# Performance work log

Hardware: AMD Instinct MI355X
Metric: run time of the kernel (lower is better)

## Reference

```python
import jax, jax.numpy as jnp
from jax import lax
import numpy as np

B = 2; C = 128; H = 128; W = 128; NPIX = H * W
HTH = 184; HTW = 180; NBINS = HTH * HTW
NSPH = 16384; KHT = 8; KSPH = 16
N0, N1, N2 = 1024, 256, 64
K0, K1, K2 = 8, 8, 8
EPS = 1e-5


def setup_inputs() -> dict:
    key = jax.random.key(0)
    ks = jax.random.split(key, 24)
    f32 = jnp.float32
    inp = {}
    inp["image"] = jax.random.normal(ks[0], (B, C, H, W), f32)
    inp["bn_gamma"] = jnp.ones((C,), f32)
    inp["bn_beta"] = jnp.zeros((C,), f32)
    inp["ht_idx"] = jax.random.randint(ks[1], (NBINS, KHT), 0, NPIX, jnp.int32)
    inp["ht_w"] = jax.random.uniform(ks[2], (NBINS, KHT), f32)
    inp["w_htconv"] = jax.random.normal(ks[3], (3, 3, C, C), f32) / np.sqrt(9.0 * C)
    inp["htbn_gamma"] = jnp.ones((C,), f32)
    inp["htbn_beta"] = jnp.zeros((C,), f32)
    inp["sph_idx"] = jax.random.randint(ks[4], (NSPH, KSPH), 0, NBINS, jnp.int32)
    inp["sph_w"] = jax.random.uniform(ks[5], (NSPH, KSPH), f32)
    inp["w_sc"] = jax.random.normal(ks[6], (3, 64, C), f32) / np.sqrt(1.0 * C)
    inp["b_sc"] = jnp.zeros((3, 64), f32)
    inp["scbn_gamma"] = jnp.ones((3, 64), f32)
    inp["scbn_beta"] = jnp.zeros((3, 64), f32)
    inp["dgcn_w"] = jax.random.normal(ks[7], (3, 4, 128, 64), f32) / np.sqrt(128.0)
    inp["dgcn_b"] = jnp.zeros((3, 4, 64), f32)
    inp["dgcn_hw"] = jax.random.normal(ks[8], (3, 64), f32) / 8.0
    inp["dgcn_hb"] = jnp.zeros((3,), f32)
    inp["ind0"] = jax.random.randint(ks[9], (B, N0), 0, NSPH, jnp.int32)
    inp["ind1"] = jax.random.randint(ks[10], (B, 3, N1), 0, NSPH, jnp.int32)
    inp["ind2"] = jax.random.randint(ks[11], (B, 3, N2), 0, NSPH, jnp.int32)
    # kNN-style edges: structured centers (each node repeated k times), random neighbors
    c0 = jnp.tile(jnp.repeat(jnp.arange(N0, dtype=jnp.int32), K0)[None], (B, 1))
    inp["edge0"] = jnp.stack([c0, jax.random.randint(ks[12], (B, N0 * K0), 0, N0, jnp.int32)], 1)
    c1 = jnp.broadcast_to(jnp.repeat(jnp.arange(N1, dtype=jnp.int32), K1)[None, None], (B, 3, N1 * K1))
    inp["edge1"] = jnp.stack([c1, jax.random.randint(ks[13], (B, 3, N1 * K1), 0, N1, jnp.int32)], 2)
    c2 = jnp.broadcast_to(jnp.repeat(jnp.arange(N2, dtype=jnp.int32), K2)[None, None], (B, 3, N2 * K2))
    inp["edge2"] = jnp.stack([c2, jax.random.randint(ks[14], (B, 3, N2 * K2), 0, N2, jnp.int32)], 2)
    inp["target0"] = jax.random.randint(ks[15], (B, N0), 0, 2, jnp.int32)
    inp["target1"] = jax.random.randint(ks[16], (B * 3, N1), 0, 2, jnp.int32)
    inp["target2"] = jax.random.randint(ks[17], (B * 3, N2), 0, 2, jnp.int32)
    return inp


def _bn2d(x, g, b):
    m = x.mean((0, 2, 3), keepdims=True)
    v = x.var((0, 2, 3), keepdims=True)
    return g[None, :, None, None] * (x - m) * lax.rsqrt(v + EPS) + b[None, :, None, None]


def _sphere(x_htf, sph_idx, sph_w, ind):
    # x_htf: [B,C,NBINS]; ind: [B,S] -> weighted gather of HT bins per sphere node
    mi = sph_idx[ind]          # [B,S,K]
    mw = sph_w[ind]            # [B,S,K]
    g = jax.vmap(lambda xb, ib: xb[:, ib])(x_htf, mi)   # [B,C,S,K]
    return (g * mw[:, None]).sum(-1)                    # [B,C,S]


def _sconv(x, w, b, g, be):
    # 1x1 conv [B,C,S]->[B,64,S] + BN1d (batch stats) + ReLU
    y = jnp.einsum('oc,bcs->bos', w, x) + b[None, :, None]
    m = y.mean((0, 2), keepdims=True)
    v = y.var((0, 2), keepdims=True)
    return jax.nn.relu(g[None, :, None] * (y - m) * lax.rsqrt(v + EPS) + be[None, :, None])


def _dgcn(x, edge, ws, bs, hw, hb, n, k):
    # x: [Bg,n,64]; edge: [Bg,2,n*k] (row0=center, row1=neighbor); 4 EdgeConv layers
    for i in range(4):
        xc = jnp.take_along_axis(x, edge[:, 0, :, None], axis=1)   # [Bg,n*k,Cin]
        xn = jnp.take_along_axis(x, edge[:, 1, :, None], axis=1)
        h = jax.nn.relu(jnp.concatenate([xc, xn - xc], -1) @ ws[i] + bs[i])
        x = h.reshape(x.shape[0], n, k, -1).max(2)                 # max over neighbors
    return x @ hw + hb                                             # [Bg,n] logits


def _bce(logits, target):
    t = target.astype(logits.dtype)
    l = jnp.maximum(logits, 0.0) - logits * t + jnp.log1p(jnp.exp(-jnp.abs(logits)))
    pos = t > 0.5
    npos = jnp.maximum(pos.sum(), 1).astype(l.dtype)
    nneg = jnp.maximum((~pos).sum(), 1).astype(l.dtype)
    return jnp.where(pos, l, 0.0).sum() / npos, jnp.where(pos, 0.0, l).sum() / nneg


def _forward(image, bn_gamma, bn_beta, ht_idx, ht_w, w_htconv, htbn_gamma, htbn_beta,
             sph_idx, sph_w, w_sc, b_sc, scbn_gamma, scbn_beta,
             dgcn_w, dgcn_b, dgcn_hw, dgcn_hb,
             ind0, ind1, ind2, edge0, edge1, edge2, target0, target1, target2):
    x = jax.nn.relu(_bn2d(image, bn_gamma, bn_beta))
    xf = x.reshape(B, C, NPIX)
    # Hough voting: each HT bin accumulates KHT weighted pixels
    ht = (xf[:, :, ht_idx] * ht_w).sum(-1).reshape(B, C, HTH, HTW)
    hc = lax.conv_general_dilated(ht, w_htconv, (1, 1), 'SAME',
                                  dimension_numbers=('NCHW', 'HWIO', 'NCHW'))
    x_htf = jax.nn.relu(_bn2d(hc, htbn_gamma, htbn_beta)).reshape(B, C, NBINS)

    # scale 0
    x0 = _sconv(_sphere(x_htf, sph_idx, sph_w, ind0),
                w_sc[0], b_sc[0], scbn_gamma[0], scbn_beta[0]).transpose(0, 2, 1)
    x0 = _dgcn(x0, edge0, dgcn_w[0], dgcn_b[0], dgcn_hw[0], dgcn_hb[0], N0, K0)   # [B,N0]
    # scale 1 (3 vanishing-point branches folded into batch)
    x1 = _sconv(_sphere(x_htf, sph_idx, sph_w, ind1.reshape(B, -1)),
                w_sc[1], b_sc[1], scbn_gamma[1], scbn_beta[1]).transpose(0, 2, 1)
    x1 = _dgcn(x1.reshape(B * 3, N1, 64), edge1.reshape(B * 3, 2, N1 * K1),
               dgcn_w[1], dgcn_b[1], dgcn_hw[1], dgcn_hb[1], N1, K1)              # [B*3,N1]
    # scale 2
    x2 = _sconv(_sphere(x_htf, sph_idx, sph_w, ind2.reshape(B, -1)),
                w_sc[2], b_sc[2], scbn_gamma[2], scbn_beta[2]).transpose(0, 2, 1)
    x2 = _dgcn(x2.reshape(B * 3, N2, 64), edge2.reshape(B * 3, 2, N2 * K2),
               dgcn_w[2], dgcn_b[2], dgcn_hw[2], dgcn_hb[2], N2, K2)              # [B*3,N2]

    lp0, ln0 = _bce(x0, target0)
    lp1, ln1 = _bce(x1, target1)
    lp2, ln2 = _bce(x2, target2)
    losses = jnp.stack([lp0, ln0, lp1, ln1, lp2, ln2])
    preds = jnp.concatenate([jax.nn.sigmoid(x0).reshape(B, -1),
                             jax.nn.sigmoid(x1).reshape(B, -1),
                             jax.nn.sigmoid(x2).reshape(B, -1)], axis=1)
    return losses, preds


def reference(image, bn_gamma, bn_beta, ht_idx, ht_w, w_htconv, htbn_gamma, htbn_beta,
              sph_idx, sph_w, w_sc, b_sc, scbn_gamma, scbn_beta,
              dgcn_w, dgcn_b, dgcn_hw, dgcn_hb,
              ind0, ind1, ind2, edge0, edge1, edge2, target0, target1, target2):
    return _forward(image, bn_gamma, bn_beta, ht_idx, ht_w, w_htconv, htbn_gamma, htbn_beta,
                    sph_idx, sph_w, w_sc, b_sc, scbn_gamma, scbn_beta,
                    dgcn_w, dgcn_b, dgcn_hw, dgcn_hb,
                    ind0, ind1, ind2, edge0, edge1, edge2, target0, target1, target2)
```

## Files before the change

kernel.cpp:

```cpp
#include <hip/hip_runtime.h>
#include <math.h>

#define B_ 2
#define C_ 128
#define NPIX_ 16384
#define HTH_ 184
#define HTW_ 180
#define NBINS_ 33120
#define PH_ 186
#define PW_ 184
#define NPB_ 1984
#define TOTN_ 3968
#define EPS_ 1e-5f

#define ST_HC_SUM 0
#define ST_HC_SQ  128
#define ST_SC_SUM 256
#define ST_SC_SQ  448
#define ST_LOSS   640
#define ST_TICKET 652
#define ST_IMG_S1 1472
#define ST_IMG_S2 1600

typedef __attribute__((ext_vector_type(8))) short v8s;
typedef __attribute__((ext_vector_type(4))) float v4f;

__device__ inline unsigned short f2b(float f) {
  unsigned u = __builtin_bit_cast(unsigned, f);
  unsigned r = u + 0x7fffu + ((u >> 16) & 1u);
  return (unsigned short)(r >> 16);
}
__device__ inline float b2f(unsigned short u) {
  unsigned v = ((unsigned)u) << 16;
  return __builtin_bit_cast(float, v);
}

__global__ void kprep0(const float* __restrict__ w, const float* __restrict__ dw,
                       const float* __restrict__ wsc,
                       unsigned short* __restrict__ wtb, unsigned short* __restrict__ dwb,
                       unsigned short* __restrict__ swb,
                       unsigned* __restrict__ htb2, const float* __restrict__ img,
                       float* __restrict__ st) {
  int bid = blockIdx.x;
  int tid = threadIdx.x;
  if (bid < 1612) {
    int idx = bid*256 + tid;
    if (idx < 147456) {
      int tap = idx >> 14, z = idx & 16383;
      int j = z & 7, lane = (z >> 3) & 63, nt = (z >> 9) & 7, kt = (z >> 12) & 3;
      int l = lane & 15, q = lane >> 4;
      int co = nt*16 + l, ci = kt*32 + q*8 + j;
      wtb[idx] = f2b(w[(tap*C_ + ci)*C_ + co]);
    } else if (idx < 245760) {
      int i2 = idx - 147456;
      int sl = i2 >> 13, z = i2 & 8191;
      int j = z & 7, lane = (z >> 3) & 63, nt = (z >> 9) & 3, kt = (z >> 11) & 3;
      int l = lane & 15, q = lane >> 4;
      int co = nt*16 + l, cc = kt*32 + q*8 + j;
      dwb[i2] = f2b(dw[(sl*128 + cc)*64 + co]);
    } else if (idx < 270336) {
      int i3 = idx - 245760;
      int s = i3 >> 13, z = i3 & 8191;
      int j = z & 7, lane = (z >> 3) & 63, nt = (z >> 9) & 3, kt = (z >> 11) & 3;
      int l = lane & 15, q = lane >> 4;
      int co = nt*16 + l, cc = kt*32 + q*8 + j;
      swb[i3] = f2b(wsc[(s*64 + co)*128 + cc]);
    } else if (idx < 412672) {
      int i = idx - 270336;
      int d = i & 63;
      int cell = i >> 6;
      int b = cell / 1112, j = cell % 1112;
      int y, x;
      if (j < 184) { y = 0; x = j; }
      else if (j < 368) { y = 185; x = j - 184; }
      else { int c = j - 368; int xi = c / 186; y = c % 186; x = xi == 0 ? 0 : 180 + xi; }
      htb2[((size_t)(b*PH_ + y)*PW_ + x)*64 + d] = 0u;
    }
  } else {
    int kb = bid - 1612;
    int c = kb >> 3, chunk = kb & 7;
    float s1 = 0.f, s2 = 0.f;
    for (int i = chunk*4096 + tid; i < (chunk+1)*4096; i += 256) {
      int b = i >> 14, p = i & (NPIX_-1);
      float v = img[((size_t)(b*C_ + c))*NPIX_ + p];
      s1 += v; s2 += v*v;
    }
    __shared__ float r1[256], r2[256];
    r1[tid] = s1; r2[tid] = s2; __syncthreads();
    for (int off = 128; off; off >>= 1) {
      if (tid < off) { r1[tid] += r1[tid+off]; r2[tid] += r2[tid+off]; }
      __syncthreads();
    }
    if (tid == 0) {
      atomicAdd(&st[ST_IMG_S1 + c], r1[0]);
      atomicAdd(&st[ST_IMG_S2 + c], r2[0]);
    }
  }
}

__global__ void k2_bnrelu_t(const float* __restrict__ img, const float* __restrict__ st,
                            const float* __restrict__ g, const float* __restrict__ be,
                            unsigned short* __restrict__ xt) {
  __shared__ float tile[32*65];
  __shared__ float ash[32], dsh[32];
  int p0 = blockIdx.x*64, c0 = blockIdx.y*32, b = blockIdx.z;
  int tid = threadIdx.x;
  if (tid < 32) {
    int c = c0 + tid;
    float n = (float)(B_*NPIX_);
    float m = st[ST_IMG_S1+c]/n;
    float var = st[ST_IMG_S2+c]/n - m*m;
    float a = g[c]*rsqrtf(var + EPS_);
    ash[tid] = a; dsh[tid] = be[c] - a*m;
  }
  __syncthreads();
  for (int r = 0; r < 8; r++) {
    int flat = tid + r*256;
    int row = flat >> 6, col = flat & 63;
    float v = img[((size_t)(b*C_ + c0 + row))*NPIX_ + p0 + col];
    tile[row*65 + col] = fmaxf(ash[row]*v + dsh[row], 0.f);
  }
  __syncthreads();
  for (int r = 0; r < 4; r++) {
    int flat = (tid + r*256)*2;
    int pl = flat >> 5, cl = flat & 31;
    unsigned lo = f2b(tile[cl*65 + pl]);
    unsigned hi = f2b(tile[(cl+1)*65 + pl]);
    *(unsigned*)&xt[((size_t)b*NPIX_ + p0 + pl)*C_ + c0 + cl] = lo | (hi << 16);
  }
}

__global__ void k3_hough(const unsigned* __restrict__ xt2, const int* __restrict__ hidx,
                         const float* __restrict__ hwt, unsigned* __restrict__ htb2) {
  int tid = threadIdx.x;
  int wv = __builtin_amdgcn_readfirstlane(tid >> 6);
  int lane = tid & 63;
  int b = blockIdx.y;
  int bin0 = blockIdx.x*16 + wv*4;
  const unsigned* base = xt2 + (size_t)b*NPIX_*64 + lane;
  unsigned dv[4][8];
  #pragma unroll
  for (int i = 0; i < 4; i++) {
    #pragma unroll
    for (int k = 0; k < 8; k++) {
      int p = hidx[(bin0+i)*8 + k];
      dv[i][k] = base[(size_t)p*64];
    }
  }
  #pragma unroll
  for (int i = 0; i < 4; i++) {
    int bin = bin0 + i;
    float acc0 = 0.f, acc1 = 0.f;
    #pragma unroll
    for (int k = 0; k < 8; k++) {
      float w = hwt[bin*8 + k];
      acc0 += w * b2f((unsigned short)(dv[i][k] & 0xffff));
      acc1 += w * b2f((unsigned short)(dv[i][k] >> 16));
    }
    int y = bin / HTW_, x = bin - y*HTW_;
    htb2[((size_t)(b*PH_ + y + 1)*PW_ + (x+1))*64 + lane] =
        (unsigned)f2b(acc0) | (((unsigned)f2b(acc1)) << 16);
  }
}

__global__ __launch_bounds__(256, 3) void k4_mfma(
    const unsigned short* __restrict__ htb, const unsigned short* __restrict__ wtb,
    unsigned short* __restrict__ hcb, float* __restrict__ st) {
  __shared__ char smem[32768];
  int tid = threadIdx.x;
  int wav = tid >> 6, lane = tid & 63;
  int quad = lane >> 4, l16 = lane & 15;
  int b = blockIdx.y;
  int p0 = blockIdx.x*128 + wav*32;
  size_t ab[2];
  #pragma unroll
  for (int t = 0; t < 2; t++) {
    int px = p0 + t*16 + l16; if (px > NBINS_-1) px = NBINS_-1;
    int y = px / HTW_, x = px % HTW_;
    ab[t] = (((size_t)(b*PH_ + y))*PW_ + x)*C_ + quad*8;
  }
  v4f acc[2][8];
  #pragma unroll
  for (int t = 0; t < 2; t++)
    #pragma unroll
    for (int nt = 0; nt < 8; nt++) acc[t][nt] = (v4f){0,0,0,0};

  for (int tap = 0; tap < 9; tap++) {
    __syncthreads();
    const uint4* src = (const uint4*)(wtb + tap*16384);
    uint4* dst = (uint4*)smem;
    #pragma unroll
    for (int s = 0; s < 8; s++) dst[tid + s*256] = src[tid + s*256];
    __syncthreads();
    int dy = tap/3, dx = tap - dy*3;
    int toff = (dy*PW_ + dx)*C_;
    v8s a[2][4];
    #pragma unroll
    for (int t = 0; t < 2; t++)
      #pragma unroll
      for (int kt = 0; kt < 4; kt++)
        a[t][kt] = *(const v8s*)&htb[ab[t] + toff + kt*32];
    #pragma unroll
    for (int kt = 0; kt < 4; kt++) {
      #pragma unroll
      for (int nt = 0; nt < 8; nt++) {
        v8s bf = *(const v8s*)(smem + ((((kt*8 + nt)*64) + lane) << 4));
        acc[0][nt] = __builtin_amdgcn_mfma_f32_16x16x32_bf16(a[0][kt], bf, acc[0][nt], 0, 0, 0);
        acc[1][nt] = __builtin_amdgcn_mfma_f32_16x16x32_bf16(a[1][kt], bf, acc[1][nt], 0, 0, 0);
      }
    }
  }
  __syncthreads();
  float* red = (float*)smem;
  float s1[8], s2[8];
  #pragma unroll
  for (int nt = 0; nt < 8; nt++) { s1[nt] = 0.f; s2[nt] = 0.f; }
  #pragma unroll
  for (int t = 0; t < 2; t++) {
    int pbase = p0 + t*16 + quad*4;
    #pragma unroll
    for (int nt = 0; nt < 8; nt++) {
      int co = nt*16 + l16;
      #pragma unroll
      for (int reg = 0; reg < 4; reg++) {
        int po = pbase + reg;
        if (po < NBINS_) {
          float v = acc[t][nt][reg];
          hcb[((size_t)b*NBINS_ + po)*C_ + co] = f2b(v);
          s1[nt] += v; s2[nt] += v*v;
        }
      }
    }
  }
  int slot = wav*4 + quad;
  #pragma unroll
  for (int nt = 0; nt < 8; nt++) red[(nt*16 + l16)*17 + slot] = s1[nt];
  __syncthreads();
  if (tid < 128) {
    float s = 0.f;
    #pragma unroll
    for (int k = 0; k < 16; k++) s += red[tid*17 + k];
    atomicAdd(&st[ST_HC_SUM + tid], s);
  }
  __syncthreads();
  #pragma unroll
  for (int nt = 0; nt < 8; nt++) red[(nt*16 + l16)*17 + slot] = s2[nt];
  __syncthreads();
  if (tid < 128) {
    float s = 0.f;
    #pragma unroll
    for (int k = 0; k < 16; k++) s += red[tid*17 + k];
    atomicAdd(&st[ST_HC_SQ + tid], s);
  }
}

__global__ __launch_bounds__(256) void k67_sphconv(
    const unsigned* __restrict__ hcb2, const float* __restrict__ g, const float* __restrict__ be,
    const int* __restrict__ sph_idx, const float* __restrict__ sph_w,
    const int* __restrict__ ind0, const int* __restrict__ ind1, const int* __restrict__ ind2,
    const unsigned short* __restrict__ swb, const float* __restrict__ b_sc,
    float* __restrict__ y, float* __restrict__ st) {
  __shared__ unsigned short E[16*136];
  int tid = threadIdx.x;
  int gn0 = blockIdx.x*8;
  int nb0 = gn0 % NPB_;
  int s = nb0 < 1024 ? 0 : (nb0 < 1792 ? 1 : 2);
  int wv = tid >> 6, lane = tid & 63;
  int quad = lane >> 4, l16 = lane & 15;
  {
    int c0 = lane*2, c1 = c0 + 1;
    float n = (float)(B_*NBINS_);
    float m0 = st[ST_HC_SUM + c0]/n, m1 = st[ST_HC_SUM + c1]/n;
    float va0 = st[ST_HC_SQ + c0]/n - m0*m0, va1 = st[ST_HC_SQ + c1]/n - m1*m1;
    float a0 = g[c0]*rsqrtf(va0 + EPS_), a1 = g[c1]*rsqrtf(va1 + EPS_);
    float d0 = be[c0] - a0*m0, d1 = be[c1] - a1*m1;
    #pragma unroll
    for (int i = 0; i < 2; i++) {
      int node_l = wv*2 + i;
      int gn = gn0 + node_l;
      int b = gn / NPB_, nb = gn % NPB_;
      int v;
      if (nb < 1024) v = ind0[b*1024 + nb];
      else if (nb < 1792) v = ind1[b*768 + nb - 1024];
      else v = ind2[b*192 + nb - 1792];
      v = __builtin_amdgcn_readfirstlane(v);
      const unsigned* base = hcb2 + (size_t)b*NBINS_*64 + lane;
      float acc0 = 0.f, acc1 = 0.f;
      #pragma unroll
      for (int k = 0; k < 16; k++) {
        int mi = sph_idx[v*16 + k];
        float mw = sph_w[v*16 + k];
        unsigned dv = base[(size_t)mi*64];
        acc0 += mw * fmaxf(a0*b2f((unsigned short)(dv & 0xffff)) + d0, 0.f);
        acc1 += mw * fmaxf(a1*b2f((unsigned short)(dv >> 16)) + d1, 0.f);
      }
      unsigned lo = f2b(acc0), hi = f2b(acc1);
      *(unsigned*)&E[node_l*136 + c0] = lo | (hi << 16);
    }
  }
  __syncthreads();
  v4f acc = (v4f){0,0,0,0};
  const unsigned short* wb = swb + s*8192 + wv*512;
  #pragma unroll
  for (int kt = 0; kt < 4; kt++) {
    v8s a = *(const v8s*)&E[l16*136 + quad*8 + kt*32];
    v8s bf = *(const v8s*)&wb[kt*2048 + lane*8];
    acc = __builtin_amdgcn_mfma_f32_16x16x32_bf16(a, bf, acc, 0, 0, 0);
  }
  float bias = b_sc[s*64 + wv*16 + l16];
  float s1 = 0.f, s2 = 0.f;
  #pragma unroll
  for (int reg = 0; reg < 4; reg++) {
    int row = quad*4 + reg;
    if (quad < 2) {
      float val = acc[reg] + bias;
      y[(size_t)(gn0 + row)*64 + wv*16 + l16] = val;
      s1 += val; s2 += val*val;
    }
  }
  s1 += __shfl_xor(s1, 16);
  s2 += __shfl_xor(s2, 16);
  if (quad == 0) {
    atomicAdd(&st[ST_SC_SUM + s*64 + wv*16 + l16], s1);
    atomicAdd(&st[ST_SC_SQ  + s*64 + wv*16 + l16], s2);
  }
}

__global__ __launch_bounds__(256) void k10_dgcn(
    const void* __restrict__ xin_, unsigned short* __restrict__ xout,
    const int* __restrict__ edge0, const int* __restrict__ edge1, const int* __restrict__ edge2,
    const unsigned short* __restrict__ dwb, const float* __restrict__ db,
    const float* __restrict__ st, const float* __restrict__ scg, const float* __restrict__ scb,
    int layer, int usebn) {
  __shared__ unsigned short E[64*136];
  __shared__ float ash[64], dsh[64];
  int tid = threadIdx.x;
  int bid = blockIdx.x;
  int s, node_base, le_blk, span; const int* ec;
  if (bid < 256) {
    s = 0; int b = bid >> 7; node_base = b*NPB_; le_blk = (bid & 127)*64;
    span = 8192; ec = edge0 + b*2*8192;
  } else if (bid < 448) {
    int j = bid - 256; s = 1; int seg = j >> 5; int b = seg/3, vp = seg%3;
    node_base = b*NPB_ + 1024 + vp*256; le_blk = (j & 31)*64;
    span = 2048; ec = edge1 + ((b*3+vp)*2)*2048;
  } else {
    int j = bid - 448; s = 2; int seg = j >> 3; int b = seg/3, vp = seg%3;
    node_base = b*NPB_ + 1792 + vp*64; le_blk = (j & 7)*64;
    span = 512; ec = edge2 + ((b*3+vp)*2)*512;
  }
  const int* en = ec + span;
  if (usebn) {
    if (tid < 64) {
      float n = s==0 ? 2048.f : (s==1 ? 1536.f : 384.f);
      float m = st[ST_SC_SUM + s*64 + tid]/n;
      float var = st[ST_SC_SQ + s*64 + tid]/n - m*m;
      float a = scg[s*64 + tid]*rsqrtf(var + EPS_);
      ash[tid] = a; dsh[tid] = scb[s*64 + tid] - a*m;
    }
    __syncthreads();
  }
  {
    int e_l = tid >> 2, part = tid & 3;
    int h = part >> 1, cb = (part & 1)*32;
    int e = le_blk + e_l;
    int ci = ec[e], ni = en[e];
    if (usebn) {
      const float* xc = (const float*)xin_ + (size_t)(node_base + ci)*64 + cb;
      const float* xn = (const float*)xin_ + (size_t)(node_base + ni)*64 + cb;
      float4 xc4[8], xn4[8];
      #pragma unroll
      for (int q = 0; q < 8; q++) xc4[q] = *(const float4*)&xc[q*4];
      if (h) {
        #pragma unroll
        for (int q = 0; q < 8; q++) xn4[q] = *(const float4*)&xn[q*4];
      }
      #pragma unroll
      for (int c8 = 0; c8 < 32; c8 += 8) {
        v8s pk;
        #pragma unroll
        for (int j = 0; j < 8; j++) {
          int cl = c8 + j;
          int c = cb + cl;
          float xcv = ((const float*)xc4)[cl];
          float vc = fmaxf(ash[c]*xcv + dsh[c], 0.f);
          float val = vc;
          if (h) {
            float xnv = ((const float*)xn4)[cl];
            val = fmaxf(ash[c]*xnv + dsh[c], 0.f) - vc;
          }
          pk[j] = (short)f2b(val);
        }
        *(v8s*)&E[e_l*136 + h*64 + cb + c8] = pk;
      }
    } else {
      const unsigned short* xc = (const unsigned short*)xin_ + (size_t)(node_base + ci)*64 + cb;
      const unsigned short* xn = (const unsigned short*)xin_ + (size_t)(node_base + ni)*64 + cb;
      #pragma unroll
      for (int c8 = 0; c8 < 32; c8 += 8) {
        v8s vc8 = *(const v8s*)&xc[c8];
        v8s pk = vc8;
        if (h) {
          v8s vn8 = *(const v8s*)&xn[c8];
          #pragma unroll
          for (int j = 0; j < 8; j++)
            pk[j] = (short)f2b(b2f((unsigned short)vn8[j]) - b2f((unsigned short)vc8[j]));
        }
        *(v8s*)&E[e_l*136 + h*64 + cb + c8] = pk;
      }
    }
  }
  __syncthreads();
  int wave = tid >> 6, lane = tid & 63;
  int quad = lane >> 4, l16 = lane & 15;
  const unsigned short* wb = dwb + (size_t)(s*4 + layer)*8192;
  v4f acc[4];
  #pragma unroll
  for (int nt = 0; nt < 4; nt++) acc[nt] = (v4f){0,0,0,0};
  #pragma unroll
  for (int kt = 0; kt < 4; kt++) {
    v8s a = *(const v8s*)&E[(wave*16 + l16)*136 + quad*8 + kt*32];
    #pragma unroll
    for (int nt = 0; nt < 4; nt++) {
      v8s bf = *(const v8s*)&wb[((kt*4 + nt)*64 + lane)*8];
      acc[nt] = __builtin_amdgcn_mfma_f32_16x16x32_bf16(a, bf, acc[nt], 0, 0, 0);
    }
  }
  #pragma unroll
  for (int nt = 0; nt < 4; nt++) {
    float bias = db[(s*4 + layer)*64 + nt*16 + l16];
    float m = fmaxf(fmaxf(acc[nt][0], acc[nt][1]), fmaxf(acc[nt][2], acc[nt][3]));
    m = fmaxf(m + bias, 0.f);
    float other = __shfl_xor(m, 16);
    m = fmaxf(m, other);
    if ((quad & 1) == 0) {
      int node_l = wave*2 + (quad >> 1);
      xout[(size_t)(node_base + (le_blk >> 3) + node_l)*64 + nt*16 + l16] = f2b(m);
    }
  }
}

__global__ __launch_bounds__(256) void k11_head(
    const unsigned short* __restrict__ x, const float* __restrict__ hw, const float* __restrict__ hb,
    const int* __restrict__ t0, const int* __restrict__ t1, const int* __restrict__ t2,
    float* __restrict__ out, float* __restrict__ st) {
  __shared__ float shw[192];
  int tid = threadIdx.x;
  if (tid < 192) shw[tid] = hw[tid];
  __syncthreads();
  int gn = blockIdx.x*256 + tid;
  bool valid = gn < TOTN_;
  int g = valid ? gn : TOTN_-1;
  int b = g / NPB_, nb = g % NPB_;
  int s, tg;
  if (nb < 1024) { s = 0; tg = t0[b*1024 + nb]; }
  else if (nb < 1792) { s = 1; int j = nb-1024; tg = t1[(b*3 + (j>>8))*256 + (j&255)]; }
  else { s = 2; int j = nb-1792; tg = t2[(b*3 + (j>>6))*64 + (j&63)]; }
  const unsigned short* row = x + (size_t)g*64;
  float logit = hb[s];
  #pragma unroll
  for (int c8 = 0; c8 < 64; c8 += 8) {
    v8s v = *(const v8s*)&row[c8];
    #pragma unroll
    for (int j = 0; j < 8; j++)
      logit += b2f((unsigned short)v[j]) * shw[s*64 + c8 + j];
  }
  if (valid) out[6 + gn] = 1.f / (1.f + expf(-logit));
  float tf = (float)tg;
  float l = fmaxf(logit, 0.f) - logit*tf + log1pf(expf(-fabsf(logit)));
  float sp = (valid && tg) ? l : 0.f;
  float sn = (valid && !tg) ? l : 0.f;
  float cp = (valid && tg) ? 1.f : 0.f;
  float cn = (valid && !tg) ? 1.f : 0.f;
  for (int off = 32; off; off >>= 1) {
    sp += __shfl_down(sp, off);
    sn += __shfl_down(sn, off);
    cp += __shfl_down(cp, off);
    cn += __shfl_down(cn, off);
  }
  if ((tid & 63) == 0) {
    atomicAdd(&st[ST_LOSS + s*4 + 0], sp);
    atomicAdd(&st[ST_LOSS + s*4 + 1], sn);
    atomicAdd(&st[ST_LOSS + s*4 + 2], cp);
    atomicAdd(&st[ST_LOSS + s*4 + 3], cn);
  }
  __syncthreads();
  __threadfence();
  if (tid == 0) {
    unsigned t = (unsigned)atomicAdd(&st[ST_TICKET], 1.f);
    if (t >= 15) {
      #pragma unroll
      for (int i = 0; i < 6; i++) {
        int sc = i >> 1; int pos = !(i & 1);
        float sum = atomicAdd(&st[ST_LOSS + sc*4 + (pos ? 0 : 1)], 0.f);
        float cnt = atomicAdd(&st[ST_LOSS + sc*4 + (pos ? 2 : 3)], 0.f);
        out[i] = sum / fmaxf(cnt, 1.f);
      }
    }
  }
}

extern "C" void kernel_launch(void* const* d_in, const int* in_sizes, int n_in,
                              void* d_out, int out_size, void* d_ws, size_t ws_size,
                              hipStream_t stream) {
  const float* image  = (const float*)d_in[0];
  const float* bn_g   = (const float*)d_in[1];
  const float* bn_b   = (const float*)d_in[2];
  const int*   ht_idx = (const int*)  d_in[3];
  const float* ht_w   = (const float*)d_in[4];
  const float* w_conv = (const float*)d_in[5];
  const float* htbn_g = (const float*)d_in[6];
  const float* htbn_b = (const float*)d_in[7];
  const int*   sph_idx= (const int*)  d_in[8];
  const float* sph_w  = (const float*)d_in[9];
  const float* w_sc   = (const float*)d_in[10];
  const float* b_sc   = (const float*)d_in[11];
  const float* scbn_g = (const float*)d_in[12];
  const float* scbn_b = (const float*)d_in[13];
  const float* dgcn_w = (const float*)d_in[14];
  const float* dgcn_b = (const float*)d_in[15];
  const float* dgcn_hw= (const float*)d_in[16];
  const float* dgcn_hb= (const float*)d_in[17];
  const int*   ind0   = (const int*)  d_in[18];
  const int*   ind1   = (const int*)  d_in[19];
  const int*   ind2   = (const int*)  d_in[20];
  const int*   edge0  = (const int*)  d_in[21];
  const int*   edge1  = (const int*)  d_in[22];
  const int*   edge2  = (const int*)  d_in[23];
  const int*   t0     = (const int*)  d_in[24];
  const int*   t1     = (const int*)  d_in[25];
  const int*   t2     = (const int*)  d_in[26];
  float* out = (float*)d_out;

  char* ws = (char*)d_ws;
  unsigned short* x_t   = (unsigned short*)(ws);
  unsigned short* htb   = (unsigned short*)(ws +  8388608);
  unsigned short* hcb   = (unsigned short*)(ws + 25911296);
  unsigned short* wtb   = (unsigned short*)(ws + 42868736);
  unsigned short* dwb   = (unsigned short*)(ws + 43163648);
  unsigned short* swb   = (unsigned short*)(ws + 43360256);
  float*          y_sc  = (float*)(ws + 43409408);
  unsigned short* xdgA  = (unsigned short*)(ws + 44425216);
  unsigned short* xdgB  = (unsigned short*)(ws + 44933120);
  float*          st    = (float*)(ws + 45441024);

  hipMemsetAsync(st, 0, 1728*sizeof(float), stream);
  kprep0<<<2636, 256, 0, stream>>>(w_conv, dgcn_w, w_sc, wtb, dwb, swb, (unsigned*)htb, image, st);
  k2_bnrelu_t<<<dim3(256,4,2), 256, 0, stream>>>(image, st, bn_g, bn_b, x_t);
  k3_hough<<<dim3(NBINS_/16, B_), 256, 0, stream>>>((const unsigned*)x_t, ht_idx, ht_w, (unsigned*)htb);
  k4_mfma<<<dim3(259, 2), 256, 0, stream>>>(htb, wtb, hcb, st);
  k67_sphconv<<<TOTN_/8, 256, 0, stream>>>((const unsigned*)hcb, htbn_g, htbn_b, sph_idx, sph_w,
                                           ind0, ind1, ind2, swb, b_sc, y_sc, st);
  k10_dgcn<<<496, 256, 0, stream>>>((const void*)y_sc, xdgA, edge0, edge1, edge2, dwb, dgcn_b, st, scbn_g, scbn_b, 0, 1);
  k10_dgcn<<<496, 256, 0, stream>>>((const void*)xdgA, xdgB, edge0, edge1, edge2, dwb, dgcn_b, st, scbn_g, scbn_b, 1, 0);
  k10_dgcn<<<496, 256, 0, stream>>>((const void*)xdgB, xdgA, edge0, edge1, edge2, dwb, dgcn_b, st, scbn_g, scbn_b, 2, 0);
  k10_dgcn<<<496, 256, 0, stream>>>((const void*)xdgA, xdgB, edge0, edge1, edge2, dwb, dgcn_b, st, scbn_g, scbn_b, 3, 0);
  k11_head<<<16, 256, 0, stream>>>(xdgB, dgcn_hw, dgcn_hb, t0, t1, t2, out, st);
}
```

Baseline: 239.3 us.

## Fuse sphere conv, DGCN layers and head into one persistent kernel with grid barriers

New measurement: 725.5 us. 3.03x slower.

```diff
diff --git a/kernel.cpp b/kernel.cpp
--- a/kernel.cpp
+++ b/kernel.cpp
@@ -19,8 +19,9 @@
 #define ST_SC_SQ  448
 #define ST_LOSS   640
 #define ST_TICKET 652
-#define ST_IMG_S1 1472
-#define ST_IMG_S2 1600
+#define ST_BAR    656
+#define ST_IMG_P1 704
+#define ST_IMG_P2 1728
 
 typedef __attribute__((ext_vector_type(8))) short v8s;
 typedef __attribute__((ext_vector_type(4))) float v4f;
@@ -33,6 +34,18 @@
 __device__ inline float b2f(unsigned short u) {
   unsigned v = ((unsigned)u) << 16;
   return __builtin_bit_cast(float, v);
+}
+
+__device__ inline void gbar(int* bar, int idx, int nb) {
+  __syncthreads();
+  __threadfence();
+  if (threadIdx.x == 0) {
+    __hip_atomic_fetch_add(&bar[idx], 1, __ATOMIC_ACQ_REL, __HIP_MEMORY_SCOPE_AGENT);
+    while (__hip_atomic_load(&bar[idx], __ATOMIC_ACQUIRE, __HIP_MEMORY_SCOPE_AGENT) < nb)
+      __builtin_amdgcn_s_sleep(1);
+  }
+  __syncthreads();
+  __threadfence();
 }
 
 __global__ void kprep0(const float* __restrict__ w, const float* __restrict__ dw,
@@ -76,7 +89,7 @@
       else { int c = j - 368; int xi = c / 186; y = c % 186; x = xi == 0 ? 0 : 180 + xi; }
       htb2[((size_t)(b*PH_ + y)*PW_ + x)*64 + d] = 0u;
     }
-  } else {
+  } else if (bid < 2636) {
     int kb = bid - 1612;
     int c = kb >> 3, chunk = kb & 7;
     float s1 = 0.f, s2 = 0.f;
@@ -92,9 +105,11 @@
       __syncthreads();
     }
     if (tid == 0) {
-      atomicAdd(&st[ST_IMG_S1 + c], r1[0]);
-      atomicAdd(&st[ST_IMG_S2 + c], r2[0]);
-    }
+      st[ST_IMG_P1 + chunk*128 + c] = r1[0];
+      st[ST_IMG_P2 + chunk*128 + c] = r2[0];
+    }
+  } else {
+    for (int i = tid; i < 672; i += 256) st[i] = 0.f;
   }
 }
 
@@ -107,9 +122,15 @@
   int tid = threadIdx.x;
   if (tid < 32) {
     int c = c0 + tid;
+    float s1 = 0.f, s2 = 0.f;
+    #pragma unroll
+    for (int ch = 0; ch < 8; ch++) {
+      s1 += st[ST_IMG_P1 + ch*128 + c];
+      s2 += st[ST_IMG_P2 + ch*128 + c];
+    }
     float n = (float)(B_*NPIX_);
-    float m = st[ST_IMG_S1+c]/n;
-    float var = st[ST_IMG_S2+c]/n - m*m;
+    float m = s1/n;
+    float var = s2/n - m*m;
     float a = g[c]*rsqrtf(var + EPS_);
     ash[tid] = a; dsh[tid] = be[c] - a*m;
   }
@@ -163,15 +184,16 @@
   }
 }
 
-__global__ __launch_bounds__(256, 3) void k4_mfma(
+__global__ __launch_bounds__(256, 4) void k4_mfma(
     const unsigned short* __restrict__ htb, const unsigned short* __restrict__ wtb,
     unsigned short* __restrict__ hcb, float* __restrict__ st) {
   __shared__ char smem[32768];
   int tid = threadIdx.x;
   int wav = tid >> 6, lane = tid & 63;
   int quad = lane >> 4, l16 = lane & 15;
+  int ph = wav & 1, ch = wav >> 1;
   int b = blockIdx.y;
-  int p0 = blockIdx.x*128 + wav*32;
+  int p0 = blockIdx.x*64 + ph*32;
   size_t ab[2];
   #pragma unroll
   for (int t = 0; t < 2; t++) {
@@ -179,11 +201,11 @@
     int y = px / HTW_, x = px % HTW_;
     ab[t] = (((size_t)(b*PH_ + y))*PW_ + x)*C_ + quad*8;
   }
-  v4f acc[2][8];
+  v4f acc[2][4];
   #pragma unroll
   for (int t = 0; t < 2; t++)
     #pragma unroll
-    for (int nt = 0; nt < 8; nt++) acc[t][nt] = (v4f){0,0,0,0};
+    for (int nt = 0; nt < 4; nt++) acc[t][nt] = (v4f){0,0,0,0};
 
   for (int tap = 0; tap < 9; tap++) {
     __syncthreads();
@@ -203,8 +225,8 @@
     #pragma unroll
     for (int kt = 0; kt < 4; kt++) {
       #pragma unroll
-      for (int nt = 0; nt < 8; nt++) {
-        v8s bf = *(const v8s*)(smem + ((((kt*8 + nt)*64) + lane) << 4));
+      for (int nt = 0; nt < 4; nt++) {
+        v8s bf = *(const v8s*)(smem + ((((kt*8 + ch*4 + nt)*64) + lane) << 4));
         acc[0][nt] = __builtin_amdgcn_mfma_f32_16x16x32_bf16(a[0][kt], bf, acc[0][nt], 0, 0, 0);
         acc[1][nt] = __builtin_amdgcn_mfma_f32_16x16x32_bf16(a[1][kt], bf, acc[1][nt], 0, 0, 0);
       }
@@ -212,15 +234,13 @@
   }
   __syncthreads();
   float* red = (float*)smem;
-  float s1[8], s2[8];
-  #pragma unroll
-  for (int nt = 0; nt < 8; nt++) { s1[nt] = 0.f; s2[nt] = 0.f; }
+  float s1[4] = {0,0,0,0}, s2[4] = {0,0,0,0};
   #pragma unroll
   for (int t = 0; t < 2; t++) {
     int pbase = p0 + t*16 + quad*4;
     #pragma unroll
-    for (int nt = 0; nt < 8; nt++) {
-      int co = nt*16 + l16;
+    for (int nt = 0; nt < 4; nt++) {
+      int co = ch*64 + nt*16 + l16;
       #pragma unroll
       for (int reg = 0; reg < 4; reg++) {
         int po = pbase + reg;
@@ -232,110 +252,111 @@
       }
     }
   }
-  int slot = wav*4 + quad;
-  #pragma unroll
-  for (int nt = 0; nt < 8; nt++) red[(nt*16 + l16)*17 + slot] = s1[nt];
+  int slot = ph*4 + quad;
+  #pragma unroll
+  for (int nt = 0; nt < 4; nt++) red[(ch*64 + nt*16 + l16)*9 + slot] = s1[nt];
   __syncthreads();
   if (tid < 128) {
     float s = 0.f;
     #pragma unroll
-    for (int k = 0; k < 16; k++) s += red[tid*17 + k];
+    for (int k = 0; k < 8; k++) s += red[tid*9 + k];
     atomicAdd(&st[ST_HC_SUM + tid], s);
   }
   __syncthreads();
   #pragma unroll
-  for (int nt = 0; nt < 8; nt++) red[(nt*16 + l16)*17 + slot] = s2[nt];
+  for (int nt = 0; nt < 4; nt++) red[(ch*64 + nt*16 + l16)*9 + slot] = s2[nt];
   __syncthreads();
   if (tid < 128) {
     float s = 0.f;
     #pragma unroll
-    for (int k = 0; k < 16; k++) s += red[tid*17 + k];
+    for (int k = 0; k < 8; k++) s += red[tid*9 + k];
     atomicAdd(&st[ST_HC_SQ + tid], s);
   }
 }
 
-__global__ __launch_bounds__(256) void k67_sphconv(
+__global__ __launch_bounds__(256, 2) void kmega(
     const unsigned* __restrict__ hcb2, const float* __restrict__ g, const float* __restrict__ be,
     const int* __restrict__ sph_idx, const float* __restrict__ sph_w,
     const int* __restrict__ ind0, const int* __restrict__ ind1, const int* __restrict__ ind2,
     const unsigned short* __restrict__ swb, const float* __restrict__ b_sc,
-    float* __restrict__ y, float* __restrict__ st) {
-  __shared__ unsigned short E[16*136];
-  int tid = threadIdx.x;
-  int gn0 = blockIdx.x*8;
-  int nb0 = gn0 % NPB_;
-  int s = nb0 < 1024 ? 0 : (nb0 < 1792 ? 1 : 2);
-  int wv = tid >> 6, lane = tid & 63;
-  int quad = lane >> 4, l16 = lane & 15;
-  {
-    int c0 = lane*2, c1 = c0 + 1;
-    float n = (float)(B_*NBINS_);
-    float m0 = st[ST_HC_SUM + c0]/n, m1 = st[ST_HC_SUM + c1]/n;
-    float va0 = st[ST_HC_SQ + c0]/n - m0*m0, va1 = st[ST_HC_SQ + c1]/n - m1*m1;
-    float a0 = g[c0]*rsqrtf(va0 + EPS_), a1 = g[c1]*rsqrtf(va1 + EPS_);
-    float d0 = be[c0] - a0*m0, d1 = be[c1] - a1*m1;
-    #pragma unroll
-    for (int i = 0; i < 2; i++) {
-      int node_l = wv*2 + i;
-      int gn = gn0 + node_l;
-      int b = gn / NPB_, nb = gn % NPB_;
-      int v;
-      if (nb < 1024) v = ind0[b*1024 + nb];
-      else if (nb < 1792) v = ind1[b*768 + nb - 1024];
-      else v = ind2[b*192 + nb - 1792];
-      v = __builtin_amdgcn_readfirstlane(v);
-      const unsigned* base = hcb2 + (size_t)b*NBINS_*64 + lane;
-      float acc0 = 0.f, acc1 = 0.f;
-      #pragma unroll
-      for (int k = 0; k < 16; k++) {
-        int mi = sph_idx[v*16 + k];
-        float mw = sph_w[v*16 + k];
-        unsigned dv = base[(size_t)mi*64];
-        acc0 += mw * fmaxf(a0*b2f((unsigned short)(dv & 0xffff)) + d0, 0.f);
-        acc1 += mw * fmaxf(a1*b2f((unsigned short)(dv >> 16)) + d1, 0.f);
-      }
-      unsigned lo = f2b(acc0), hi = f2b(acc1);
-      *(unsigned*)&E[node_l*136 + c0] = lo | (hi << 16);
-    }
-  }
-  __syncthreads();
-  v4f acc = (v4f){0,0,0,0};
-  const unsigned short* wb = swb + s*8192 + wv*512;
-  #pragma unroll
-  for (int kt = 0; kt < 4; kt++) {
-    v8s a = *(const v8s*)&E[l16*136 + quad*8 + kt*32];
-    v8s bf = *(const v8s*)&wb[kt*2048 + lane*8];
-    acc = __builtin_amdgcn_mfma_f32_16x16x32_bf16(a, bf, acc, 0, 0, 0);
-  }
-  float bias = b_sc[s*64 + wv*16 + l16];
-  float s1 = 0.f, s2 = 0.f;
-  #pragma unroll
-  for (int reg = 0; reg < 4; reg++) {
-    int row = quad*4 + reg;
-    if (quad < 2) {
-      float val = acc[reg] + bias;
-      y[(size_t)(gn0 + row)*64 + wv*16 + l16] = val;
-      s1 += val; s2 += val*val;
-    }
-  }
-  s1 += __shfl_xor(s1, 16);
-  s2 += __shfl_xor(s2, 16);
-  if (quad == 0) {
-    atomicAdd(&st[ST_SC_SUM + s*64 + wv*16 + l16], s1);
-    atomicAdd(&st[ST_SC_SQ  + s*64 + wv*16 + l16], s2);
-  }
-}
-
-__global__ __launch_bounds__(256) void k10_dgcn(
-    const void* __restrict__ xin_, unsigned short* __restrict__ xout,
     const int* __restrict__ edge0, const int* __restrict__ edge1, const int* __restrict__ edge2,
     const unsigned short* __restrict__ dwb, const float* __restrict__ db,
-    const float* __restrict__ st, const float* __restrict__ scg, const float* __restrict__ scb,
-    int layer, int usebn) {
+    const float* __restrict__ scg, const float* __restrict__ scb,
+    const float* __restrict__ hw, const float* __restrict__ hb,
+    const int* __restrict__ t0, const int* __restrict__ t1, const int* __restrict__ t2,
+    float* __restrict__ y_sc, unsigned short* __restrict__ xdgA, unsigned short* __restrict__ xdgB,
+    float* __restrict__ out, float* __restrict__ st) {
   __shared__ unsigned short E[64*136];
   __shared__ float ash[64], dsh[64];
   int tid = threadIdx.x;
   int bid = blockIdx.x;
+  int* bar = (int*)&st[ST_BAR];
+  int wv = tid >> 6, lane = tid & 63;
+  int quad = lane >> 4, l16 = lane & 15;
+
+  {
+    int gn0 = bid*8;
+    int nb0 = gn0 % NPB_;
+    int s = nb0 < 1024 ? 0 : (nb0 < 1792 ? 1 : 2);
+    {
+      int c0 = lane*2, c1 = c0 + 1;
+      float n = (float)(B_*NBINS_);
+      float m0 = st[ST_HC_SUM + c0]/n, m1 = st[ST_HC_SUM + c1]/n;
+      float va0 = st[ST_HC_SQ + c0]/n - m0*m0, va1 = st[ST_HC_SQ + c1]/n - m1*m1;
+      float a0 = g[c0]*rsqrtf(va0 + EPS_), a1 = g[c1]*rsqrtf(va1 + EPS_);
+      float d0 = be[c0] - a0*m0, d1 = be[c1] - a1*m1;
+      #pragma unroll
+      for (int i = 0; i < 2; i++) {
+        int node_l = wv*2 + i;
+        int gn = gn0 + node_l;
+        int b = gn / NPB_, nb = gn % NPB_;
+        int v;
+        if (nb < 1024) v = ind0[b*1024 + nb];
+        else if (nb < 1792) v = ind1[b*768 + nb - 1024];
+        else v = ind2[b*192 + nb - 1792];
+        v = __builtin_amdgcn_readfirstlane(v);
+        const unsigned* base = hcb2 + (size_t)b*NBINS_*64 + lane;
+        float acc0 = 0.f, acc1 = 0.f;
+        #pragma unroll
+        for (int k = 0; k < 16; k++) {
+          int mi = sph_idx[v*16 + k];
+          float mw = sph_w[v*16 + k];
+          unsigned dv = base[(size_t)mi*64];
+          acc0 += mw * fmaxf(a0*b2f((unsigned short)(dv & 0xffff)) + d0, 0.f);
+          acc1 += mw * fmaxf(a1*b2f((unsigned short)(dv >> 16)) + d1, 0.f);
+        }
+        unsigned lo = f2b(acc0), hi = f2b(acc1);
+        *(unsigned*)&E[node_l*136 + c0] = lo | (hi << 16);
+      }
+    }
+    __syncthreads();
+    v4f acc = (v4f){0,0,0,0};
+    const unsigned short* wb = swb + s*8192 + wv*512;
+    #pragma unroll
+    for (int kt = 0; kt < 4; kt++) {
+      v8s a = *(const v8s*)&E[l16*136 + quad*8 + kt*32];
+      v8s bf = *(const v8s*)&wb[kt*2048 + lane*8];
+      acc = __builtin_amdgcn_mfma_f32_16x16x32_bf16(a, bf, acc, 0, 0, 0);
+    }
+    float bias = b_sc[s*64 + wv*16 + l16];
+    float s1 = 0.f, s2 = 0.f;
+    #pragma unroll
+    for (int reg = 0; reg < 4; reg++) {
+      int row = quad*4 + reg;
+      if (quad < 2) {
+        float val = acc[reg] + bias;
+        y_sc[(size_t)(gn0 + row)*64 + wv*16 + l16] = val;
+        s1 += val; s2 += val*val;
+      }
+    }
+    s1 += __shfl_xor(s1, 16);
+    s2 += __shfl_xor(s2, 16);
+    if (quad == 0) {
+      atomicAdd(&st[ST_SC_SUM + s*64 + wv*16 + l16], s1);
+      atomicAdd(&st[ST_SC_SQ  + s*64 + wv*16 + l16], s2);
+    }
+  }
+
   int s, node_base, le_blk, span; const int* ec;
   if (bid < 256) {
     s = 0; int b = bid >> 7; node_base = b*NPB_; le_blk = (bid & 127)*64;
@@ -350,151 +371,158 @@
     span = 512; ec = edge2 + ((b*3+vp)*2)*512;
   }
   const int* en = ec + span;
-  if (usebn) {
-    if (tid < 64) {
-      float n = s==0 ? 2048.f : (s==1 ? 1536.f : 384.f);
-      float m = st[ST_SC_SUM + s*64 + tid]/n;
-      float var = st[ST_SC_SQ + s*64 + tid]/n - m*m;
-      float a = scg[s*64 + tid]*rsqrtf(var + EPS_);
-      ash[tid] = a; dsh[tid] = scb[s*64 + tid] - a*m;
-    }
-    __syncthreads();
-  }
+
+  for (int layer = 0; layer < 4; layer++) {
+    gbar(bar, layer, 496);
+    if (layer == 0) {
+      if (tid < 64) {
+        float n = s==0 ? 2048.f : (s==1 ? 1536.f : 384.f);
+        float m = st[ST_SC_SUM + s*64 + tid]/n;
+        float var = st[ST_SC_SQ + s*64 + tid]/n - m*m;
+        float a = scg[s*64 + tid]*rsqrtf(var + EPS_);
+        ash[tid] = a; dsh[tid] = scb[s*64 + tid] - a*m;
+      }
+      __syncthreads();
+    }
+    const void* xin_ = layer == 0 ? (const void*)y_sc
+                     : (layer == 1 ? (const void*)xdgA
+                     : (layer == 2 ? (const void*)xdgB : (const void*)xdgA));
+    unsigned short* xout = (layer & 1) ? xdgB : xdgA;
+    if (layer == 2) xout = xdgA; else if (layer == 0) xout = xdgA; else xout = xdgB;
+    {
+      int e_l = tid >> 2, part = tid & 3;
+      int h = part >> 1, cb = (part & 1)*32;
+      int e = le_blk + e_l;
+      int ci = ec[e], ni = en[e];
+      if (layer == 0) {
+        const float* xc = (const float*)xin_ + (size_t)(node_base + ci)*64 + cb;
+        const float* xn = (const float*)xin_ + (size_t)(node_base + ni)*64 + cb;
+        float4 xc4[8], xn4[8];
+        #pragma unroll
+        for (int q = 0; q < 8; q++) xc4[q] = *(const float4*)&xc[q*4];
+        if (h) {
+          #pragma unroll
+          for (int q = 0; q < 8; q++) xn4[q] = *(const float4*)&xn[q*4];
+        }
+        #pragma unroll
+        for (int c8 = 0; c8 < 32; c8 += 8) {
+          v8s pk;
+          #pragma unroll
+          for (int j = 0; j < 8; j++) {
+            int cl = c8 + j;
+            int c = cb + cl;
+            float xcv = ((const float*)xc4)[cl];
+            float vc = fmaxf(ash[c]*xcv + dsh[c], 0.f);
+            float val = vc;
+            if (h) {
+              float xnv = ((const float*)xn4)[cl];
+              val = fmaxf(ash[c]*xnv + dsh[c], 0.f) - vc;
+            }
+            pk[j] = (short)f2b(val);
+          }
+          *(v8s*)&E[e_l*136 + h*64 + cb + c8] = pk;
+        }
+      } else {
+        const unsigned short* xc = (const unsigned short*)xin_ + (size_t)(node_base + ci)*64 + cb;
+        const unsigned short* xn = (const unsigned short*)xin_ + (size_t)(node_base + ni)*64 + cb;
+        #pragma unroll
+        for (int c8 = 0; c8 < 32; c8 += 8) {
+          v8s vc8 = *(const v8s*)&xc[c8];
+          v8s pk = vc8;
+          if (h) {
+            v8s vn8 = *(const v8s*)&xn[c8];
+            #pragma unroll
+            for (int j = 0; j < 8; j++)
+              pk[j] = (short)f2b(b2f((unsigned short)vn8[j]) - b2f((unsigned short)vc8[j]));
+          }
+          *(v8s*)&E[e_l*136 + h*64 + cb + c8] = pk;
+        }
+      }
+    }
+    __syncthreads();
+    const unsigned short* wb = dwb + (size_t)(s*4 + layer)*8192;
+    v4f acc[4];
+    #pragma unroll
+    for (int nt = 0; nt < 4; nt++) acc[nt] = (v4f){0,0,0,0};
+    #pragma unroll
+    for (int kt = 0; kt < 4; kt++) {
+      v8s a = *(const v8s*)&E[(wv*16 + l16)*136 + quad*8 + kt*32];
+      #pragma unroll
+      for (int nt = 0; nt < 4; nt++) {
+        v8s bf = *(const v8s*)&wb[((kt*4 + nt)*64 + lane)*8];
+        acc[nt] = __builtin_amdgcn_mfma_f32_16x16x32_bf16(a, bf, acc[nt], 0, 0, 0);
+      }
+    }
+    #pragma unroll
+    for (int nt = 0; nt < 4; nt++) {
+      float bias = db[(s*4 + layer)*64 + nt*16 + l16];
+      float m = fmaxf(fmaxf(acc[nt][0], acc[nt][1]), fmaxf(acc[nt][2], acc[nt][3]));
+      m = fmaxf(m + bias, 0.f);
+      float other = __shfl_xor(m, 16);
+      m = fmaxf(m, other);
+      if ((quad & 1) == 0) {
+        int node_l = wv*2 + (quad >> 1);
+        xout[(size_t)(node_base + (le_blk >> 3) + node_l)*64 + nt*16 + l16] = f2b(m);
+      }
+    }
+    __syncthreads();
+  }
+
+  gbar(bar, 4, 496);
+  if (bid >= 16) return;
+
   {
-    int e_l = tid >> 2, part = tid & 3;
-    int h = part >> 1, cb = (part & 1)*32;
-    int e = le_blk + e_l;
-    int ci = ec[e], ni = en[e];
-    if (usebn) {
-      const float* xc = (const float*)xin_ + (size_t)(node_base + ci)*64 + cb;
-      const float* xn = (const float*)xin_ + (size_t)(node_base + ni)*64 + cb;
-      float4 xc4[8], xn4[8];
+    __shared__ float shw[192];
+    if (tid < 192) shw[tid] = hw[tid];
+    __syncthreads();
+    int gn = bid*256 + tid;
+    bool valid = gn < TOTN_;
+    int gg = valid ? gn : TOTN_-1;
+    int b = gg / NPB_, nb = gg % NPB_;
+    int sc_, tg;
+    if (nb < 1024) { sc_ = 0; tg = t0[b*1024 + nb]; }
+    else if (nb < 1792) { sc_ = 1; int j = nb-1024; tg = t1[(b*3 + (j>>8))*256 + (j&255)]; }
+    else { sc_ = 2; int j = nb-1792; tg = t2[(b*3 + (j>>6))*64 + (j&63)]; }
+    const unsigned short* row = xdgB + (size_t)gg*64;
+    float logit = hb[sc_];
+    #pragma unroll
+    for (int c8 = 0; c8 < 64; c8 += 8) {
+      v8s v = *(const v8s*)&row[c8];
       #pragma unroll
-      for (int q = 0; q < 8; q++) xc4[q] = *(const float4*)&xc[q*4];
-      if (h) {
+      for (int j = 0; j < 8; j++)
+        logit += b2f((unsigned short)v[j]) * shw[sc_*64 + c8 + j];
+    }
+    if (valid) out[6 + gn] = 1.f / (1.f + expf(-logit));
+    float tf = (float)tg;
+    float l = fmaxf(logit, 0.f) - logit*tf + log1pf(expf(-fabsf(logit)));
+    float sp = (valid && tg) ? l : 0.f;
+    float sn = (valid && !tg) ? l : 0.f;
+    float cp = (valid && tg) ? 1.f : 0.f;
+    float cn = (valid && !tg) ? 1.f : 0.f;
+    for (int off = 32; off; off >>= 1) {
+      sp += __shfl_down(sp, off);
+      sn += __shfl_down(sn, off);
+      cp += __shfl_down(cp, off);
+      cn += __shfl_down(cn, off);
+    }
+    if ((tid & 63) == 0) {
+      atomicAdd(&st[ST_LOSS + sc_*4 + 0], sp);
+      atomicAdd(&st[ST_LOSS + sc_*4 + 1], sn);
+      atomicAdd(&st[ST_LOSS + sc_*4 + 2], cp);
+      atomicAdd(&st[ST_LOSS + sc_*4 + 3], cn);
+    }
+    __syncthreads();
+    __threadfence();
+    if (tid == 0) {
+      unsigned t = (unsigned)atomicAdd(&st[ST_TICKET], 1.f);
+      if (t >= 15) {
         #pragma unroll
-        for (int q = 0; q < 8; q++) xn4[q] = *(const float4*)&xn[q*4];
-      }
-      #pragma unroll
-      for (int c8 = 0; c8 < 32; c8 += 8) {
-        v8s pk;
-        #pragma unroll
-        for (int j = 0; j < 8; j++) {
-          int cl = c8 + j;
-          int c = cb + cl;
-          float xcv = ((const float*)xc4)[cl];
-          float vc = fmaxf(ash[c]*xcv + dsh[c], 0.f);
-          float val = vc;
-          if (h) {
-            float xnv = ((const float*)xn4)[cl];
-            val = fmaxf(ash[c]*xnv + dsh[c], 0.f) - vc;
-          }
-          pk[j] = (short)f2b(val);
+        for (int i = 0; i < 6; i++) {
+          int sc2 = i >> 1; int pos = !(i & 1);
+          float sum = atomicAdd(&st[ST_LOSS + sc2*4 + (pos ? 0 : 1)], 0.f);
+          float cnt = atomicAdd(&st[ST_LOSS + sc2*4 + (pos ? 2 : 3)], 0.f);
+          out[i] = sum / fmaxf(cnt, 1.f);
         }
-        *(v8s*)&E[e_l*136 + h*64 + cb + c8] = pk;
-      }
-    } else {
-      const unsigned short* xc = (const unsigned short*)xin_ + (size_t)(node_base + ci)*64 + cb;
-      const unsigned short* xn = (const unsigned short*)xin_ + (size_t)(node_base + ni)*64 + cb;
-      #pragma unroll
-      for (int c8 = 0; c8 < 32; c8 += 8) {
-        v8s vc8 = *(const v8s*)&xc[c8];
-        v8s pk = vc8;
-        if (h) {
-          v8s vn8 = *(const v8s*)&xn[c8];
-          #pragma unroll
-          for (int j = 0; j < 8; j++)
-            pk[j] = (short)f2b(b2f((unsigned short)vn8[j]) - b2f((unsigned short)vc8[j]));
-        }
-        *(v8s*)&E[e_l*136 + h*64 + cb + c8] = pk;
-      }
-    }
-  }
-  __syncthreads();
-  int wave = tid >> 6, lane = tid & 63;
-  int quad = lane >> 4, l16 = lane & 15;
-  const unsigned short* wb = dwb + (size_t)(s*4 + layer)*8192;
-  v4f acc[4];
-  #pragma unroll
-  for (int nt = 0; nt < 4; nt++) acc[nt] = (v4f){0,0,0,0};
-  #pragma unroll
-  for (int kt = 0; kt < 4; kt++) {
-    v8s a = *(const v8s*)&E[(wave*16 + l16)*136 + quad*8 + kt*32];
-    #pragma unroll
-    for (int nt = 0; nt < 4; nt++) {
-      v8s bf = *(const v8s*)&wb[((kt*4 + nt)*64 + lane)*8];
-      acc[nt] = __builtin_amdgcn_mfma_f32_16x16x32_bf16(a, bf, acc[nt], 0, 0, 0);
-    }
-  }
-  #pragma unroll
-  for (int nt = 0; nt < 4; nt++) {
-    float bias = db[(s*4 + layer)*64 + nt*16 + l16];
-    float m = fmaxf(fmaxf(acc[nt][0], acc[nt][1]), fmaxf(acc[nt][2], acc[nt][3]));
-    m = fmaxf(m + bias, 0.f);
-    float other = __shfl_xor(m, 16);
-    m = fmaxf(m, other);
-    if ((quad & 1) == 0) {
-      int node_l = wave*2 + (quad >> 1);
-      xout[(size_t)(node_base + (le_blk >> 3) + node_l)*64 + nt*16 + l16] = f2b(m);
-    }
-  }
-}
-
-__global__ __launch_bounds__(256) void k11_head(
-    const unsigned short* __restrict__ x, const float* __restrict__ hw, const float* __restrict__ hb,
-    const int* __restrict__ t0, const int* __restrict__ t1, const int* __restrict__ t2,
-    float* __restrict__ out, float* __restrict__ st) {
-  __shared__ float shw[192];
-  int tid = threadIdx.x;
-  if (tid < 192) shw[tid] = hw[tid];
-  __syncthreads();
-  int gn = blockIdx.x*256 + tid;
-  bool valid = gn < TOTN_;
-  int g = valid ? gn : TOTN_-1;
-  int b = g / NPB_, nb = g % NPB_;
-  int s, tg;
-  if (nb < 1024) { s = 0; tg = t0[b*1024 + nb]; }
-  else if (nb < 1792) { s = 1; int j = nb-1024; tg = t1[(b*3 + (j>>8))*256 + (j&255)]; }
-  else { s = 2; int j = nb-1792; tg = t2[(b*3 + (j>>6))*64 + (j&63)]; }
-  const unsigned short* row = x + (size_t)g*64;
-  float logit = hb[s];
-  #pragma unroll
-  for (int c8 = 0; c8 < 64; c8 += 8) {
-    v8s v = *(const v8s*)&row[c8];
-    #pragma unroll
-    for (int j = 0; j < 8; j++)
-      logit += b2f((unsigned short)v[j]) * shw[s*64 + c8 + j];
-  }
-  if (valid) out[6 + gn] = 1.f / (1.f + expf(-logit));
-  float tf = (float)tg;
-  float l = fmaxf(logit, 0.f) - logit*tf + log1pf(expf(-fabsf(logit)));
-  float sp = (valid && tg) ? l : 0.f;
-  float sn = (valid && !tg) ? l : 0.f;
-  float cp = (valid && tg) ? 1.f : 0.f;
-  float cn = (valid && !tg) ? 1.f : 0.f;
-  for (int off = 32; off; off >>= 1) {
-    sp += __shfl_down(sp, off);
-    sn += __shfl_down(sn, off);
-    cp += __shfl_down(cp, off);
-    cn += __shfl_down(cn, off);
-  }
-  if ((tid & 63) == 0) {
-    atomicAdd(&st[ST_LOSS + s*4 + 0], sp);
-    atomicAdd(&st[ST_LOSS + s*4 + 1], sn);
-    atomicAdd(&st[ST_LOSS + s*4 + 2], cp);
-    atomicAdd(&st[ST_LOSS + s*4 + 3], cn);
-  }
-  __syncthreads();
-  __threadfence();
-  if (tid == 0) {
-    unsigned t = (unsigned)atomicAdd(&st[ST_TICKET], 1.f);
-    if (t >= 15) {
-      #pragma unroll
-      for (int i = 0; i < 6; i++) {
-        int sc = i >> 1; int pos = !(i & 1);
-        float sum = atomicAdd(&st[ST_LOSS + sc*4 + (pos ? 0 : 1)], 0.f);
-        float cnt = atomicAdd(&st[ST_LOSS + sc*4 + (pos ? 2 : 3)], 0.f);
-        out[i] = sum / fmaxf(cnt, 1.f);
       }
     }
   }
@@ -544,16 +572,13 @@
   unsigned short* xdgB  = (unsigned short*)(ws + 44933120);
   float*          st    = (float*)(ws + 45441024);
 
-  hipMemsetAsync(st, 0, 1728*sizeof(float), stream);
-  kprep0<<<2636, 256, 0, stream>>>(w_conv, dgcn_w, w_sc, wtb, dwb, swb, (unsigned*)htb, image, st);
+  kprep0<<<2637, 256, 0, stream>>>(w_conv, dgcn_w, w_sc, wtb, dwb, swb, (unsigned*)htb, image, st);
   k2_bnrelu_t<<<dim3(256,4,2), 256, 0, stream>>>(image, st, bn_g, bn_b, x_t);
   k3_hough<<<dim3(NBINS_/16, B_), 256, 0, stream>>>((const unsigned*)x_t, ht_idx, ht_w, (unsigned*)htb);
-  k4_mfma<<<dim3(259, 2), 256, 0, stream>>>(htb, wtb, hcb, st);
-  k67_sphconv<<<TOTN_/8, 256, 0, stream>>>((const unsigned*)hcb, htbn_g, htbn_b, sph_idx, sph_w,
-                                           ind0, ind1, ind2, swb, b_sc, y_sc, st);
-  k10_dgcn<<<496, 256, 0, stream>>>((const void*)y_sc, xdgA, edge0, edge1, edge2, dwb, dgcn_b, st, scbn_g, scbn_b, 0, 1);
-  k10_dgcn<<<496, 256, 0, stream>>>((const void*)xdgA, xdgB, edge0, edge1, edge2, dwb, dgcn_b, st, scbn_g, scbn_b, 1, 0);
-  k10_dgcn<<<496, 256, 0, stream>>>((const void*)xdgB, xdgA, edge0, edge1, edge2, dwb, dgcn_b, st, scbn_g, scbn_b, 2, 0);
-  k10_dgcn<<<496, 256, 0, stream>>>((const void*)xdgA, xdgB, edge0, edge1, edge2, dwb, dgcn_b, st, scbn_g, scbn_b, 3, 0);
-  k11_head<<<16, 256, 0, stream>>>(xdgB, dgcn_hw, dgcn_hb, t0, t1, t2, out, st);
-}
+  k4_mfma<<<dim3(518, 2), 256, 0, stream>>>(htb, wtb, hcb, st);
+  kmega<<<496, 256, 0, stream>>>((const unsigned*)hcb, htbn_g, htbn_b, sph_idx, sph_w,
+                                 ind0, ind1, ind2, swb, b_sc,
+                                 edge0, edge1, edge2, dwb, dgcn_b, scbn_g, scbn_b,
+                                 dgcn_hw, dgcn_hb, t0, t1, t2,
+                                 y_sc, xdgA, xdgB, out, st);
+}
```
